# Kernel tuning notes

Measured on AMD Instinct MI355X. Metric: run time of the kernel, lower is better.

## Reference

```python
import jax, jax.numpy as jnp
import numpy as np

B, N, CL = 128, 64, 64


def _lin_params(key, fan_in, fan_out):
    k1, k2 = jax.random.split(key)
    bound = 1.0 / np.sqrt(fan_in)
    w = jax.random.uniform(k1, (fan_in, fan_out), jnp.float32, -bound, bound)
    b = jax.random.uniform(k2, (fan_out,), jnp.float32, -bound, bound)
    return w, b


def setup_inputs() -> dict:
    key = jax.random.key(0)
    ks = jax.random.split(key, 12)
    cl = CL
    se_w1, se_b1 = _lin_params(ks[0], cl, cl)
    se_w2, se_b2 = _lin_params(ks[1], cl, cl)
    sd_w1, sd_b1 = _lin_params(ks[2], cl, 2 * cl)
    sd_w2, sd_b2 = _lin_params(ks[3], 2 * cl, 2 * cl)
    rc_w1, rc_b1 = _lin_params(ks[4], 2 * cl + 1, 2 * cl)
    rc_w2, rc_b2 = _lin_params(ks[5], 2 * cl, 2 * cl)
    rc_w3, rc_b3 = _lin_params(ks[6], 2 * cl, 2 * cl)
    an_w1, an_b1 = _lin_params(ks[7], 2 * cl + 1, cl)
    an_w2, an_b2 = _lin_params(ks[8], cl, 2 * cl)
    s = jax.random.normal(ks[9], (B, N, cl), jnp.float32)
    return dict(s=s,
                se_w1=se_w1, se_b1=se_b1, se_w2=se_w2, se_b2=se_b2,
                sd_w1=sd_w1, sd_b1=sd_b1, sd_w2=sd_w2, sd_b2=sd_b2,
                rc_w1=rc_w1, rc_b1=rc_b1, rc_w2=rc_w2, rc_b2=rc_b2,
                rc_w3=rc_w3, rc_b3=rc_b3,
                an_w1=an_w1, an_b1=an_b1, an_w2=an_w2, an_b2=an_b2)


def reference(s, se_w1, se_b1, se_w2, se_b2,
              sd_w1, sd_b1, sd_w2, sd_b2,
              rc_w1, rc_b1, rc_w2, rc_b2, rc_w3, rc_b3,
              an_w1, an_b1, an_w2, an_b2):
    relu = jax.nn.relu
    # state encoder: [B, N, cl]
    h = relu(relu(s @ se_w1 + se_b1) @ se_w2 + se_b2)
    Bn, Nn, cl = h.shape
    # all-pairs features [B, N, N, cl]
    a1 = jnp.broadcast_to(h[:, :, None, :], (Bn, Nn, Nn, cl))  # object_arg1
    a2 = jnp.broadcast_to(h[:, None, :, :], (Bn, Nn, Nn, cl))  # object_arg2
    dist = (a1[..., 0] - a2[..., 0]) ** 2 + (a1[..., 1] - a2[..., 1]) ** 2
    feat = jnp.concatenate([a1, a2, dist[..., None]], axis=-1)  # [B,N,N,2cl+1]
    rel = relu(relu(relu(feat @ rc_w1 + rc_b1) @ rc_w2 + rc_b2) @ rc_w3 + rc_b3)
    att = jax.nn.sigmoid(relu(feat @ an_w1 + an_b1) @ an_w2 + an_b2)
    rel_dyn = jnp.mean(rel * att, axis=2)  # [B, N, 2cl]
    self_dyn = relu(h @ sd_w1 + sd_b1) @ sd_w2 + sd_b2  # [B, N, 2cl]
    return jnp.mean(self_dyn + rel_dyn, axis=1)  # [B, 2cl]
```

## Files before the change

### kernel.cpp

```cpp
#include <hip/hip_runtime.h>
#include <math.h>

#define TPB 256

typedef unsigned short u16;
typedef __attribute__((ext_vector_type(8))) _Float16 f16x8;
typedef __attribute__((ext_vector_type(4))) float f32x4;

#define BLOB_U16 524288
#define BASE_RC_F32 327680
#define BASE_AN_F32 1376256
#define RC1P_F32 1900544
#define AN1P_F32 2949120
#define WS_NEED_BASES ((size_t)1900544 * 4)
#define WS_NEED_PRE   ((size_t)3473408 * 4)
#define RC1F 0
#define AN1F 16384
#define AN2F 24576
#define RC2F 40960
#define RC3F 73728

#define ENC_NB 512

__device__ __forceinline__ float h2f(u16 b) {
  return (float)__builtin_bit_cast(_Float16, b);
}
__device__ __forceinline__ u16 f2h_rne(float x) {
  return __builtin_bit_cast(u16, (_Float16)x);
}
__device__ __forceinline__ void split_f16(float x, u16& hi, u16& lo) {
  _Float16 h = (_Float16)x;
  hi = __builtin_bit_cast(u16, h);
  lo = __builtin_bit_cast(u16, (_Float16)(x - (float)h));
}
__device__ __forceinline__ unsigned pack_f16(float v0, float v1) {
  auto h = __builtin_amdgcn_cvt_pkrtz(v0, v1);
  return __builtin_bit_cast(unsigned, h);
}

__device__ __forceinline__ void cp_lds(float* dst, const float* src, int nfloats, int tid) {
  const float4* s4 = (const float4*)src;
  float4* d4 = (float4*)dst;
  const int n4 = nfloats >> 2;
  for (int i = tid; i < n4; i += TPB) d4[i] = s4[i];
}
__device__ __forceinline__ void ld4(float r[4], const float* p) {
  float4 v = *(const float4*)p;
  r[0] = v.x; r[1] = v.y; r[2] = v.z; r[3] = v.w;
}
__device__ __forceinline__ void ld2(float r[2], const float* p) {
  float2 v = *(const float2*)p;
  r[0] = v.x; r[1] = v.y;
}

__global__ __launch_bounds__(TPB, 3) void enc_prep_kernel(
    const float* __restrict__ s_in,
    const float* __restrict__ se_w1, const float* __restrict__ se_b1,
    const float* __restrict__ se_w2, const float* __restrict__ se_b2,
    const float* __restrict__ sd_w1, const float* __restrict__ sd_b1,
    const float* __restrict__ sd_w2, const float* __restrict__ sd_b2,
    const float* __restrict__ rc_w1, const float* __restrict__ rc_b1,
    const float* __restrict__ rc_w2, const float* __restrict__ rc_w3,
    const float* __restrict__ an_w1, const float* __restrict__ an_b1,
    const float* __restrict__ an_w2,
    u16* __restrict__ hB, u16* __restrict__ blob,
    float* __restrict__ baseRcG, float* __restrict__ baseAnG,
    float* __restrict__ rc1pG, float* __restrict__ an1pG,
    int do_bases, int do_pre,
    float* __restrict__ out) {
  if (blockIdx.x >= ENC_NB) {
    int idx = (int)(blockIdx.x - ENC_NB) * TPB + threadIdx.x;
    if (idx >= 53248) return;
    int r, base, OK, T; const float* W; int Wld, krow0, twoTerm;
    if (idx < 8192)       { r = idx;         base = RC1F; OK = 8192;  T = 8; W = rc_w1; Wld = 128; krow0 = 64; twoTerm = 1; }
    else if (idx < 12288) { r = idx - 8192;  base = AN1F; OK = 4096;  T = 4; W = an_w1; Wld = 64;  krow0 = 64; twoTerm = 1; }
    else if (idx < 20480) { r = idx - 12288; base = AN2F; OK = 8192;  T = 8; W = an_w2; Wld = 128; krow0 = 0;  twoTerm = 0; }
    else if (idx < 36864) { r = idx - 20480; base = RC2F; OK = 16384; T = 8; W = rc_w2; Wld = 128; krow0 = 0;  twoTerm = 0; }
    else                  { r = idx - 36864; base = RC3F; OK = 16384; T = 8; W = rc_w3; Wld = 128; krow0 = 0;  twoTerm = 0; }
    const int u = r & 7;
    const int lane = (r >> 3) & 63;
    const int ct = r >> 9;
    const int c = (T == 8) ? (ct >> 3) : (ct >> 2);
    const int tg = (T == 8) ? (ct & 7) : (ct & 3);
    const int o = tg * 16 + (lane & 15);
    const int k = c * 32 + (lane >> 4) * 8 + u;
    const float x = W[(krow0 + k) * Wld + o];
    if (twoTerm) {
      u16 hi, lo; split_f16(x, hi, lo);
      blob[base + r] = hi;
      blob[base + OK + r] = lo;
    } else {
      blob[base + r] = f2h_rne(x);
    }
    return;
  }

  __shared__ __align__(16) float sX[1024];
  __shared__ __align__(16) float sH1[1024];
  __shared__ __align__(16) float sT[2048];
  __shared__ __align__(16) float sW[4096];
  __shared__ float sb1[64], sb2[64], sdb1[128], sdb2[128], srb1[128], sab1[64];

  const int tid = threadIdx.x;
  const int lg = tid >> 5;
  const int og = tid & 31;
  const int b = blockIdx.x >> 2;
  const int q = blockIdx.x & 3;
  const int row0 = b * 64 + q * 16;
  const int n0 = lg * 2;

  cp_lds(sX, s_in + row0 * 64, 1024, tid);
  cp_lds(sW, se_w1, 4096, tid);
  if (tid < 64) { sb1[tid] = se_b1[tid]; sb2[tid] = se_b2[tid]; }
  else if (tid < 192) { const int o = tid - 64; sdb1[o] = sd_b1[o]; sdb2[o] = sd_b2[o]; }
  if (tid < 128) srb1[tid] = rc_b1[tid];
  else if (tid < 192) sab1[tid - 128] = an_b1[tid - 128];
  __syncthreads();

  float a2[2][2];
#pragma unroll
  for (int nn = 0; nn < 2; nn++) { a2[nn][0] = 0.f; a2[nn][1] = 0.f; }
  for (int kk = 0; kk < 64; kk += 4) {
    float xr[2][4], wr[4][2];
#pragma unroll
    for (int nn = 0; nn < 2; nn++) ld4(xr[nn], &sX[(n0 + nn) * 64 + kk]);
#pragma unroll
    for (int t = 0; t < 4; t++) ld2(wr[t], &sW[(kk + t) * 64 + og * 2]);
#pragma unroll
    for (int t = 0; t < 4; t++)
#pragma unroll
      for (int nn = 0; nn < 2; nn++) {
        a2[nn][0] = fmaf(xr[nn][t], wr[t][0], a2[nn][0]);
        a2[nn][1] = fmaf(xr[nn][t], wr[t][1], a2[nn][1]);
      }
  }
#pragma unroll
  for (int nn = 0; nn < 2; nn++) {
    float2 v;
    v.x = fmaxf(a2[nn][0] + sb1[og * 2 + 0], 0.f);
    v.y = fmaxf(a2[nn][1] + sb1[og * 2 + 1], 0.f);
    *(float2*)&sH1[(n0 + nn) * 64 + og * 2] = v;
  }
  __syncthreads();
  cp_lds(sW, se_w2, 4096, tid);
  __syncthreads();

#pragma unroll
  for (int nn = 0; nn < 2; nn++) { a2[nn][0] = 0.f; a2[nn][1] = 0.f; }
  for (int kk = 0; kk < 64; kk += 4) {
    float xr[2][4], wr[4][2];
#pragma unroll
    for (int nn = 0; nn < 2; nn++) ld4(xr[nn], &sH1[(n0 + nn) * 64 + kk]);
#pragma unroll
    for (int t = 0; t < 4; t++) ld2(wr[t], &sW[(kk + t) * 64 + og * 2]);
#pragma unroll
    for (int t = 0; t < 4; t++)
#pragma unroll
      for (int nn = 0; nn < 2; nn++) {
        a2[nn][0] = fmaf(xr[nn][t], wr[t][0], a2[nn][0]);
        a2[nn][1] = fmaf(xr[nn][t], wr[t][1], a2[nn][1]);
      }
  }
#pragma unroll
  for (int nn = 0; nn < 2; nn++) {
    float2 v;
    v.x = fmaxf(a2[nn][0] + sb2[og * 2 + 0], 0.f);
    v.y = fmaxf(a2[nn][1] + sb2[og * 2 + 1], 0.f);
    *(float2*)&sX[(n0 + nn) * 64 + og * 2] = v;
    const int off = (row0 + n0 + nn) * 64 + og * 2;
    *(ushort2*)&hB[off] = make_ushort2(f2h_rne(v.x), f2h_rne(v.y));
  }
  __syncthreads();

  float a4[2][4];
#pragma unroll
  for (int nn = 0; nn < 2; nn++)
#pragma unroll
    for (int oo = 0; oo < 4; oo++) a4[nn][oo] = 0.f;
  for (int c = 0; c < 2; c++) {
    cp_lds(sW, sd_w1 + c * 32 * 128, 4096, tid);
    __syncthreads();
    for (int kk = 0; kk < 32; kk += 4) {
      float xr[2][4], wr[4][4];
#pragma unroll
      for (int nn = 0; nn < 2; nn++) ld4(xr[nn], &sX[(n0 + nn) * 64 + c * 32 + kk]);
#pragma unroll
      for (int t = 0; t < 4; t++) ld4(wr[t], &sW[(kk + t) * 128 + og * 4]);
#pragma unroll
      for (int t = 0; t < 4; t++)
#pragma unroll
        for (int nn = 0; nn < 2; nn++)
#pragma unroll
          for (int oo = 0; oo < 4; oo++)
            a4[nn][oo] = fmaf(xr[nn][t], wr[t][oo], a4[nn][oo]);
    }
    __syncthreads();
  }
#pragma unroll
  for (int nn = 0; nn < 2; nn++) {
    float4 v;
    v.x = fmaxf(a4[nn][0] + sdb1[og * 4 + 0], 0.f);
    v.y = fmaxf(a4[nn][1] + sdb1[og * 4 + 1], 0.f);
    v.z = fmaxf(a4[nn][2] + sdb1[og * 4 + 2], 0.f);
    v.w = fmaxf(a4[nn][3] + sdb1[og * 4 + 3], 0.f);
    *(float4*)&sT[(n0 + nn) * 128 + og * 4] = v;
  }
  __syncthreads();

#pragma unroll
  for (int nn = 0; nn < 2; nn++)
#pragma unroll
    for (int oo = 0; oo < 4; oo++) a4[nn][oo] = 0.f;
  for (int c = 0; c < 4; c++) {
    cp_lds(sW, sd_w2 + c * 32 * 128, 4096, tid);
    __syncthreads();
    for (int kk = 0; kk < 32; kk += 4) {
      float xr[2][4], wr[4][4];
#pragma unroll
      for (int nn = 0; nn < 2; nn++) ld4(xr[nn], &sT[(n0 + nn) * 128 + c * 32 + kk]);
#pragma unroll
      for (int t = 0; t < 4; t++) ld4(wr[t], &sW[(kk + t) * 128 + og * 4]);
#pragma unroll
      for (int t = 0; t < 4; t++)
#pragma unroll
        for (int nn = 0; nn < 2; nn++)
#pragma unroll
          for (int oo = 0; oo < 4; oo++)
            a4[nn][oo] = fmaf(xr[nn][t], wr[t][oo], a4[nn][oo]);
    }
    __syncthreads();
  }
  float p[4];
#pragma unroll
  for (int oo = 0; oo < 4; oo++)
    p[oo] = a4[0][oo] + a4[1][oo] + 2.f * sdb2[og * 4 + oo];
  *(float4*)&sH1[lg * 128 + og * 4] = make_float4(p[0], p[1], p[2], p[3]);
  __syncthreads();
  if (tid < 128) {
    float ssum = 0.f;
#pragma unroll
    for (int g = 0; g < 8; g++) ssum += sH1[g * 128 + tid];
    atomicAdd(&out[b * 128 + tid], ssum * (1.0f / 64.0f));
  }

  if (do_bases) {
#pragma unroll
    for (int nn = 0; nn < 2; nn++)
#pragma unroll
      for (int oo = 0; oo < 4; oo++) a4[nn][oo] = 0.f;
    for (int c = 0; c < 2; c++) {
      __syncthreads();
      cp_lds(sW, rc_w1 + c * 32 * 128, 4096, tid);
      __syncthreads();
      for (int kk = 0; kk < 32; kk += 4) {
        float xr[2][4], wr[4][4];
#pragma unroll
        for (int nn = 0; nn < 2; nn++) ld4(xr[nn], &sX[(n0 + nn) * 64 + c * 32 + kk]);
#pragma unroll
        for (int t = 0; t < 4; t++) ld4(wr[t], &sW[(kk + t) * 128 + og * 4]);
#pragma unroll
        for (int t = 0; t < 4; t++)
#pragma unroll
          for (int nn = 0; nn < 2; nn++)
#pragma unroll
            for (int oo = 0; oo < 4; oo++)
              a4[nn][oo] = fmaf(xr[nn][t], wr[t][oo], a4[nn][oo]);
      }
    }
#pragma unroll
    for (int nn = 0; nn < 2; nn++) {
      float4 v;
      v.x = a4[nn][0] + srb1[og * 4 + 0];
      v.y = a4[nn][1] + srb1[og * 4 + 1];
      v.z = a4[nn][2] + srb1[og * 4 + 2];
      v.w = a4[nn][3] + srb1[og * 4 + 3];
      *(float4*)&baseRcG[(size_t)(row0 + n0 + nn) * 128 + og * 4] = v;
    }
    __syncthreads();
    cp_lds(sW, an_w1, 4096, tid);
    __syncthreads();
#pragma unroll
    for (int nn = 0; nn < 2; nn++) { a2[nn][0] = 0.f; a2[nn][1] = 0.f; }
    for (int kk = 0; kk < 64; kk += 4) {
      float xr[2][4], wr[4][2];
#pragma unroll
      for (int nn = 0; nn < 2; nn++) ld4(xr[nn], &sX[(n0 + nn) * 64 + kk]);
#pragma unroll
      for (int t = 0; t < 4; t++) ld2(wr[t], &sW[(kk + t) * 64 + og * 2]);
#pragma unroll
      for (int t = 0; t < 4; t++)
#pragma unroll
        for (int nn = 0; nn < 2; nn++) {
          a2[nn][0] = fmaf(xr[nn][t], wr[t][0], a2[nn][0]);
          a2[nn][1] = fmaf(xr[nn][t], wr[t][1], a2[nn][1]);
        }
    }
#pragma unroll
    for (int nn = 0; nn < 2; nn++) {
      float2 v;
      v.x = a2[nn][0] + sab1[og * 2 + 0];
      v.y = a2[nn][1] + sab1[og * 2 + 1];
      *(float2*)&baseAnG[(size_t)(row0 + n0 + nn) * 64 + og * 2] = v;
    }
  }

  if (do_pre) {
#pragma unroll
    for (int nn = 0; nn < 2; nn++)
#pragma unroll
      for (int oo = 0; oo < 4; oo++) a4[nn][oo] = 0.f;
    for (int c = 0; c < 2; c++) {
      __syncthreads();
      cp_lds(sW, rc_w1 + (64 + c * 32) * 128, 4096, tid);
      __syncthreads();
      for (int kk = 0; kk < 32; kk += 4) {
        float xr[2][4], wr[4][4];
#pragma unroll
        for (int nn = 0; nn < 2; nn++) ld4(xr[nn], &sX[(n0 + nn) * 64 + c * 32 + kk]);
#pragma unroll
        for (int t = 0; t < 4; t++) ld4(wr[t], &sW[(kk + t) * 128 + og * 4]);
#pragma unroll
        for (int t = 0; t < 4; t++)
#pragma unroll
          for (int nn = 0; nn < 2; nn++)
#pragma unroll
            for (int oo = 0; oo < 4; oo++)
              a4[nn][oo] = fmaf(xr[nn][t], wr[t][oo], a4[nn][oo]);
      }
    }
#pragma unroll
    for (int nn = 0; nn < 2; nn++) {
      const int jl = q * 16 + n0 + nn;
      const int addr = ((b * 8 + (og >> 2)) * 4 + (jl >> 4)) * 256 +
                       ((og & 3) * 16 + (jl & 15)) * 4;
      *(float4*)&rc1pG[addr] = make_float4(a4[nn][0], a4[nn][1], a4[nn][2], a4[nn][3]);
    }
    __syncthreads();
    cp_lds(sW, an_w1 + 64 * 64, 4096, tid);
    __syncthreads();
#pragma unroll
    for (int nn = 0; nn < 2; nn++) { a2[nn][0] = 0.f; a2[nn][1] = 0.f; }
    for (int kk = 0; kk < 64; kk += 4) {
      float xr[2][4], wr[4][2];
#pragma unroll
      for (int nn = 0; nn < 2; nn++) ld4(xr[nn], &sX[(n0 + nn) * 64 + kk]);
#pragma unroll
      for (int t = 0; t < 4; t++) ld2(wr[t], &sW[(kk + t) * 64 + og * 2]);
#pragma unroll
      for (int t = 0; t < 4; t++)
#pragma unroll
        for (int nn = 0; nn < 2; nn++) {
          a2[nn][0] = fmaf(xr[nn][t], wr[t][0], a2[nn][0]);
          a2[nn][1] = fmaf(xr[nn][t], wr[t][1], a2[nn][1]);
        }
    }
#pragma unroll
    for (int nn = 0; nn < 2; nn++) {
      const int jl = q * 16 + n0 + nn;
      const int addr = ((b * 4 + (og >> 3)) * 4 + (jl >> 4)) * 256 +
                       (((og >> 1) & 3) * 16 + (jl & 15)) * 4 + (og & 1) * 2;
      *(float2*)&an1pG[addr] = make_float2(a2[nn][0], a2[nn][1]);
    }
  }
}

template<int MT, int NCHUNK, int RSG, int TILES>
__device__ __forceinline__ void run_layer1(f32x4 (&acc)[MT][4],
    const u16* __restrict__ blobL,
    const u16* __restrict__ sB, int tg0, int quad, int l15) {
  const int lane = quad * 16 + l15;
#pragma unroll
  for (int c = 0; c < NCHUNK; ++c) {
    f16x8 Ah[MT];
#pragma unroll
    for (int t = 0; t < MT; ++t)
      Ah[t] = *(const f16x8*)(blobL + ((c * TILES + tg0 + t) * 64 + lane) * 8);
    const int slot = (4 * c + quad) ^ (l15 & 7);
    f16x8 Bh[4];
#pragma unroll
    for (int s = 0; s < 4; ++s)
      Bh[s] = *(const f16x8*)&sB[(16 * s + l15) * (RSG * 8) + slot * 8];
#pragma unroll
    for (int t = 0; t < MT; ++t)
#pragma unroll
      for (int s = 0; s < 4; ++s)
        acc[t][s] = __builtin_amdgcn_mfma_f32_16x16x32_f16(Ah[t], Bh[s], acc[t][s], 0, 0, 0);
  }
}

template<int MT, int RSG>
__device__ __forceinline__ void store_acts_pk(const f32x4 (&acc)[MT][4],
                                              u16* dst, int o0, int quad, int l15) {
#pragma unroll
  for (int t = 0; t < MT; ++t) {
    const int ob = o0 + 16 * t + quad * 4;
    const int slot = (ob >> 3) ^ (l15 & 7);
    const int e = ob & 7;
#pragma unroll
    for (int s = 0; s < 4; ++s) {
      const int j = 16 * s + l15;
      uint2 pk;
      pk.x = pack_f16(fmaxf(acc[t][s][0], 0.f), fmaxf(acc[t][s][1], 0.f));
      pk.y = pack_f16(fmaxf(acc[t][s][2], 0.f), fmaxf(acc[t][s][3], 0.f));
      *(uint2*)&dst[j * (RSG * 8) + slot * 8 + e] = pk;
    }
  }
}

__global__ __launch_bounds__(TPB, 4) void pair_mfma_kernel(
    const u16* __restrict__ hB, const u16* __restrict__ blob,
    const float* __restrict__ baseRcG, const float* __restrict__ baseAnG,
    const float* __restrict__ rc1pG, const float* __restrict__ an1pG,
    int has_bases, int has_pre,
    const float* __restrict__ rc_w1, const float* __restrict__ rc_b1,
    const float* __restrict__ rc_b2, const float* __restrict__ rc_b3,
    const float* __restrict__ an_w1, const float* __restrict__ an_b1,
    const float* __restrict__ an_b2,
    float* __restrict__ out) {
  __shared__ __align__(16) u16 sAct[64 * 128];
  __shared__ __align__(16) u16 sAn[64 * 64];
  __shared__ float sHi[64], sDist[64];
  __shared__ float sBaseRc[128], sBaseAn[64], sW1d[128], sAnd[64];
  __shared__ float sB2[128], sB3[128], sAb2[128], sRed[128];

  const int tid = threadIdx.x;
  const int w = tid >> 6, lane = tid & 63;
  const int quad = lane >> 4, l15 = lane & 15;
  const int b = blockIdx.x >> 6, i = blockIdx.x & 63;
  const int o0 = w * 32;
  const int o0a = w * 16;

  f32x4 accR[2][4];
  f32x4 accN[1][4];

  if (has_pre) {
    if (tid < 128) {
      sW1d[tid] = rc_w1[128 * 128 + tid];
      sB2[tid] = rc_b2[tid]; sB3[tid] = rc_b3[tid]; sAb2[tid] = an_b2[tid];
    } else if (tid < 192) {
      sAnd[tid - 128] = an_w1[128 * 64 + (tid - 128)];
    } else {
      const int j = tid - 192;
      const float hi0 = h2f(hB[(b * 64 + i) * 64 + 0]);
      const float hi1 = h2f(hB[(b * 64 + i) * 64 + 1]);
      const ushort2 hj = *(const ushort2*)&hB[(b * 64 + j) * 64];
      const float d0 = hi0 - h2f(hj.x), d1 = hi1 - h2f(hj.y);
      sDist[j] = d0 * d0 + d1 * d1;
    }
    if (tid < 32)
      ((float4*)sBaseRc)[tid] = ((const float4*)(baseRcG + (size_t)(b * 64 + i) * 128))[tid];
    else if (tid < 48)
      ((float4*)sBaseAn)[tid - 32] = ((const float4*)(baseAnG + (size_t)(b * 64 + i) * 64))[tid - 32];
    __syncthreads();

    float bbR[2][4], wwR[2][4], bbN[4], wwN[4];
#pragma unroll
    for (int t = 0; t < 2; ++t) {
      ld4(bbR[t], &sBaseRc[o0 + 16 * t + quad * 4]);
      ld4(wwR[t], &sW1d[o0 + 16 * t + quad * 4]);
    }
    ld4(bbN, &sBaseAn[o0a + quad * 4]);
    ld4(wwN, &sAnd[o0a + quad * 4]);
    const float* pR = rc1pG + (size_t)(b * 8 + 2 * w) * 1024 + lane * 4;
    const float* pA = an1pG + (size_t)(b * 4 + w) * 1024 + lane * 4;
#pragma unroll
    for (int s = 0; s < 4; ++s) {
      const float dj = sDist[16 * s + l15];
#pragma unroll
      for (int t = 0; t < 2; ++t) {
        const float4 pre = *(const float4*)(pR + t * 1024 + s * 256);
        f32x4 a;
        a[0] = pre.x + fmaf(dj, wwR[t][0], bbR[t][0]);
        a[1] = pre.y + fmaf(dj, wwR[t][1], bbR[t][1]);
        a[2] = pre.z + fmaf(dj, wwR[t][2], bbR[t][2]);
        a[3] = pre.w + fmaf(dj, wwR[t][3], bbR[t][3]);
        accR[t][s] = a;
      }
      const float4 pre = *(const float4*)(pA + s * 256);
      f32x4 a;
      a[0] = pre.x + fmaf(dj, wwN[0], bbN[0]);
      a[1] = pre.y + fmaf(dj, wwN[1], bbN[1]);
      a[2] = pre.z + fmaf(dj, wwN[2], bbN[2]);
      a[3] = pre.w + fmaf(dj, wwN[3], bbN[3]);
      accN[0][s] = a;
    }
    store_acts_pk<1, 8>(accN, sAn, o0a, quad, l15);
    store_acts_pk<2, 16>(accR, sAct, o0, quad, l15);
    __syncthreads();
  } else {
    {
      const float4* srcJ = (const float4*)(hB + b * 4096);
      for (int idx = tid; idx < 512; idx += TPB) {
        const int row = idx >> 3, g = idx & 7;
        *(float4*)&sAct[row * 128 + ((g ^ (row & 7)) * 8)] = srcJ[idx];
      }
    }
    if (has_bases) {
      const float4* bR = (const float4*)(baseRcG + (size_t)(b * 64 + i) * 128);
      const float4* bA = (const float4*)(baseAnG + (size_t)(b * 64 + i) * 64);
      if (tid < 32) ((float4*)sBaseRc)[tid] = bR[tid];
      else if (tid < 48) ((float4*)sBaseAn)[tid - 32] = bA[tid - 32];
    }
    if (tid < 64) sHi[tid] = h2f(hB[(b * 64 + i) * 64 + tid]);
    if (tid < 128) {
      sW1d[tid] = rc_w1[128 * 128 + tid];
      sB2[tid] = rc_b2[tid]; sB3[tid] = rc_b3[tid]; sAb2[tid] = an_b2[tid];
    } else if (tid < 192) {
      sAnd[tid - 128] = an_w1[128 * 64 + (tid - 128)];
    }
    __syncthreads();
    if (!has_bases) {
      if (tid < 128) {
        float acc = rc_b1[tid];
        for (int k = 0; k < 64; ++k) acc = fmaf(sHi[k], rc_w1[k * 128 + tid], acc);
        sBaseRc[tid] = acc;
      } else if (tid < 192) {
        const int o = tid - 128;
        float acc = an_b1[o];
        for (int k = 0; k < 64; ++k) acc = fmaf(sHi[k], an_w1[k * 64 + o], acc);
        sBaseAn[o] = acc;
      }
    }
    if (tid >= 192) {
      const int j = tid - 192;
      const int base = j * 128 + ((0 ^ (j & 7)) * 8);
      const float d0 = sHi[0] - h2f(sAct[base + 0]);
      const float d1 = sHi[1] - h2f(sAct[base + 1]);
      sDist[j] = d0 * d0 + d1 * d1;
    }
    __syncthreads();

    {
      float bbR[2][4], wwR[2][4], bbN[4], wwN[4];
#pragma unroll
      for (int t = 0; t < 2; ++t) {
        ld4(bbR[t], &sBaseRc[o0 + 16 * t + quad * 4]);
        ld4(wwR[t], &sW1d[o0 + 16 * t + quad * 4]);
      }
      ld4(bbN, &sBaseAn[o0a + quad * 4]);
      ld4(wwN, &sAnd[o0a + quad * 4]);
#pragma unroll
      for (int s = 0; s < 4; ++s) {
        const float dj = sDist[16 * s + l15];
#pragma unroll
        for (int t = 0; t < 2; ++t) {
          f32x4 a;
#pragma unroll
          for (int r = 0; r < 4; ++r) a[r] = fmaf(dj, wwR[t][r], bbR[t][r]);
          accR[t][s] = a;
        }
        f32x4 a;
#pragma unroll
        for (int r = 0; r < 4; ++r) a[r] = fmaf(dj, wwN[r], bbN[r]);
        accN[0][s] = a;
      }
    }
    {
      const int lane64 = quad * 16 + l15;
#pragma unroll
      for (int c = 0; c < 2; ++c) {
        f16x8 Ah[2], Al[2], AhN, AlN;
#pragma unroll
        for (int t = 0; t < 2; ++t) {
          const u16* p = blob + RC1F + ((c * 8 + 2 * w + t) * 64 + lane64) * 8;
          Ah[t] = *(const f16x8*)p;
          Al[t] = *(const f16x8*)(p + 8192);
        }
        {
          const u16* p = blob + AN1F + ((c * 4 + w) * 64 + lane64) * 8;
          AhN = *(const f16x8*)p;
          AlN = *(const f16x8*)(p + 4096);
        }
        const int slot = (4 * c + quad) ^ (l15 & 7);
        f16x8 Bh[4];
#pragma unroll
        for (int s = 0; s < 4; ++s)
          Bh[s] = *(const f16x8*)&sAct[(16 * s + l15) * 128 + slot * 8];
#pragma unroll
        for (int s = 0; s < 4; ++s) {
#pragma unroll
          for (int t = 0; t < 2; ++t) {
            f32x4 a = accR[t][s];
            a = __builtin_amdgcn_mfma_f32_16x16x32_f16(Ah[t], Bh[s], a, 0, 0, 0);
            a = __builtin_amdgcn_mfma_f32_16x16x32_f16(Al[t], Bh[s], a, 0, 0, 0);
            accR[t][s] = a;
          }
          f32x4 a = accN[0][s];
          a = __builtin_amdgcn_mfma_f32_16x16x32_f16(AhN, Bh[s], a, 0, 0, 0);
          a = __builtin_amdgcn_mfma_f32_16x16x32_f16(AlN, Bh[s], a, 0, 0, 0);
          accN[0][s] = a;
        }
      }
    }
    store_acts_pk<1, 8>(accN, sAn, o0a, quad, l15);
    __syncthreads();
    store_acts_pk<2, 16>(accR, sAct, o0, quad, l15);
    __syncthreads();
  }

  {
    float bb[2][4];
#pragma unroll
    for (int t = 0; t < 2; ++t) ld4(bb[t], &sB2[o0 + 16 * t + quad * 4]);
#pragma unroll
    for (int t = 0; t < 2; ++t)
#pragma unroll
      for (int s = 0; s < 4; ++s) {
        f32x4 a;
#pragma unroll
        for (int r = 0; r < 4; ++r) a[r] = bb[t][r];
        accR[t][s] = a;
      }
  }
  run_layer1<2, 4, 16, 8>(accR, blob + RC2F, sAct, 2 * w, quad, l15);
  __syncthreads();
  store_acts_pk<2, 16>(accR, sAct, o0, quad, l15);
  __syncthreads();

  f32x4 accT[2][4];
  {
    float bb[2][4];
#pragma unroll
    for (int t = 0; t < 2; ++t) ld4(bb[t], &sAb2[o0 + 16 * t + quad * 4]);
#pragma unroll
    for (int t = 0; t < 2; ++t)
#pragma unroll
      for (int s = 0; s < 4; ++s) {
        f32x4 a;
#pragma unroll
        for (int r = 0; r < 4; ++r) a[r] = bb[t][r];
        accT[t][s] = a;
      }
  }
  run_layer1<2, 2, 8, 8>(accT, blob + AN2F, sAn, 2 * w, quad, l15);
  float att[2][4][4];
#pragma unroll
  for (int t = 0; t < 2; ++t)
#pragma unroll
    for (int s = 0; s < 4; ++s)
#pragma unroll
      for (int r = 0; r < 4; ++r)
        att[t][s][r] = __builtin_amdgcn_rcpf(1.0f + __expf(-accT[t][s][r]));

  {
    float bb[2][4];
#pragma unroll
    for (int t = 0; t < 2; ++t) ld4(bb[t], &sB3[o0 + 16 * t + quad * 4]);
#pragma unroll
    for (int t = 0; t < 2; ++t)
#pragma unroll
      for (int s = 0; s < 4; ++s) {
        f32x4 a;
#pragma unroll
        for (int r = 0; r < 4; ++r) a[r] = bb[t][r];
        accR[t][s] = a;
      }
  }
  run_layer1<2, 4, 16, 8>(accR, blob + RC3F, sAct, 2 * w, quad, l15);
  float ps[2][4] = {{0.f, 0.f, 0.f, 0.f}, {0.f, 0.f, 0.f, 0.f}};
#pragma unroll
  for (int t = 0; t < 2; ++t)
#pragma unroll
    for (int s = 0; s < 4; ++s)
#pragma unroll
      for (int r = 0; r < 4; ++r) {
        const float rel = fmaxf(accR[t][s][r], 0.f);
        ps[t][r] = fmaf(rel, att[t][s][r], ps[t][r]);
      }
#pragma unroll
  for (int t = 0; t < 2; ++t)
#pragma unroll
    for (int r = 0; r < 4; ++r) {
      float v = ps[t][r];
      v += __shfl_xor(v, 1, 64);
      v += __shfl_xor(v, 2, 64);
      v += __shfl_xor(v, 4, 64);
      v += __shfl_xor(v, 8, 64);
      ps[t][r] = v;
    }
  if (l15 == 0) {
#pragma unroll
    for (int t = 0; t < 2; ++t)
#pragma unroll
      for (int r = 0; r < 4; ++r)
        sRed[o0 + 16 * t + quad * 4 + r] = ps[t][r];
  }
  __syncthreads();
  if (tid < 128)
    atomicAdd(&out[b * 128 + tid], sRed[tid] * (1.0f / 4096.0f));
}

extern "C" void kernel_launch(void* const* d_in, const int* in_sizes, int n_in,
                              void* d_out, int out_size, void* d_ws, size_t ws_size,
                              hipStream_t stream) {
  const float* s     = (const float*)d_in[0];
  const float* se_w1 = (const float*)d_in[1];
  const float* se_b1 = (const float*)d_in[2];
  const float* se_w2 = (const float*)d_in[3];
  const float* se_b2 = (const float*)d_in[4];
  const float* sd_w1 = (const float*)d_in[5];
  const float* sd_b1 = (const float*)d_in[6];
  const float* sd_w2 = (const float*)d_in[7];
  const float* sd_b2 = (const float*)d_in[8];
  const float* rc_w1 = (const float*)d_in[9];
  const float* rc_b1 = (const float*)d_in[10];
  const float* rc_w2 = (const float*)d_in[11];
  const float* rc_b2 = (const float*)d_in[12];
  const float* rc_w3 = (const float*)d_in[13];
  const float* rc_b3 = (const float*)d_in[14];
  const float* an_w1 = (const float*)d_in[15];
  const float* an_b1 = (const float*)d_in[16];
  const float* an_w2 = (const float*)d_in[17];
  const float* an_b2 = (const float*)d_in[18];
  float* out = (float*)d_out;
  u16* hB   = (u16*)d_ws;
  u16* blob = hB + BLOB_U16;
  float* baseRcG = (float*)d_ws + BASE_RC_F32;
  float* baseAnG = (float*)d_ws + BASE_AN_F32;
  float* rc1pG   = (float*)d_ws + RC1P_F32;
  float* an1pG   = (float*)d_ws + AN1P_F32;
  const int has_pre   = (ws_size >= WS_NEED_PRE) ? 1 : 0;
  const int has_bases = (ws_size >= WS_NEED_BASES) ? 1 : 0;
  (void)n_in; (void)in_sizes;

  hipMemsetAsync(d_out, 0, (size_t)out_size * sizeof(float), stream);
  enc_prep_kernel<<<ENC_NB + 208, TPB, 0, stream>>>(s, se_w1, se_b1, se_w2, se_b2,
                                           sd_w1, sd_b1, sd_w2, sd_b2,
                                           rc_w1, rc_b1, rc_w2, rc_w3,
                                           an_w1, an_b1, an_w2,
                                           hB, blob, baseRcG, baseAnG, rc1pG, an1pG,
                                           has_bases, has_pre, out);
  pair_mfma_kernel<<<8192, TPB, 0, stream>>>(hB, blob, baseRcG, baseAnG, rc1pG, an1pG,
                                             has_bases, has_pre,
                                             rc_w1, rc_b1, rc_b2, rc_b3,
                                             an_w1, an_b1, an_b2, out);
}
```

Baseline: 191.5 us.

## Rewrite encoder prep kernel with split-f16 MFMA, one block per batch

The encoder/precompute kernel previously ran scalar fp32 FMAs over 512 blocks of 16 rows each. It now uses one block per batch (128 blocks) and runs every small matmul on f16 MFMA with a hi/lo split (three MFMAs per tile) to keep near-fp32 accuracy. Weights are converted into swizzled hi/lo f16 layouts in LDS inside each block, and the self-dynamics reduction moves to wave shuffles. This trades scalar ALU work for matrix-core work, but with only 128 blocks per-block weight conversion is repeated and parallelism is lower, which may limit the gain on a kernel that is small next to the pair kernel.

```diff
diff --git a/kernel.cpp b/kernel.cpp
--- a/kernel.cpp
+++ b/kernel.cpp
@@ -4,6 +4,7 @@
 #define TPB 256
 
 typedef unsigned short u16;
+typedef unsigned int u32;
 typedef __attribute__((ext_vector_type(8))) _Float16 f16x8;
 typedef __attribute__((ext_vector_type(4))) float f32x4;
 
@@ -20,7 +21,7 @@
 #define RC2F 40960
 #define RC3F 73728
 
-#define ENC_NB 512
+#define ENC_BLOCKS 128
 
 __device__ __forceinline__ float h2f(u16 b) {
   return (float)__builtin_bit_cast(_Float16, b);
@@ -37,23 +38,132 @@
   auto h = __builtin_amdgcn_cvt_pkrtz(v0, v1);
   return __builtin_bit_cast(unsigned, h);
 }
-
-__device__ __forceinline__ void cp_lds(float* dst, const float* src, int nfloats, int tid) {
-  const float4* s4 = (const float4*)src;
-  float4* d4 = (float4*)dst;
-  const int n4 = nfloats >> 2;
-  for (int i = tid; i < n4; i += TPB) d4[i] = s4[i];
+__device__ __forceinline__ void split4(const float4 v, uint2& H, uint2& L) {
+  _Float16 h0 = (_Float16)v.x, h1 = (_Float16)v.y;
+  _Float16 h2 = (_Float16)v.z, h3 = (_Float16)v.w;
+  _Float16 l0 = (_Float16)(v.x - (float)h0), l1 = (_Float16)(v.y - (float)h1);
+  _Float16 l2 = (_Float16)(v.z - (float)h2), l3 = (_Float16)(v.w - (float)h3);
+  H.x = (u32)__builtin_bit_cast(u16, h0) | ((u32)__builtin_bit_cast(u16, h1) << 16);
+  H.y = (u32)__builtin_bit_cast(u16, h2) | ((u32)__builtin_bit_cast(u16, h3) << 16);
+  L.x = (u32)__builtin_bit_cast(u16, l0) | ((u32)__builtin_bit_cast(u16, l1) << 16);
+  L.y = (u32)__builtin_bit_cast(u16, l2) | ((u32)__builtin_bit_cast(u16, l3) << 16);
 }
 __device__ __forceinline__ void ld4(float r[4], const float* p) {
   float4 v = *(const float4*)p;
   r[0] = v.x; r[1] = v.y; r[2] = v.z; r[3] = v.w;
 }
-__device__ __forceinline__ void ld2(float r[2], const float* p) {
-  float2 v = *(const float2*)p;
-  r[0] = v.x; r[1] = v.y;
-}
-
-__global__ __launch_bounds__(TPB, 3) void enc_prep_kernel(
+
+template<int KDIM, int ODIM>
+__device__ __forceinline__ void prep_w(u16* __restrict__ hi, u16* __restrict__ lo,
+                                       const float* __restrict__ W, int tid) {
+  constexpr int N = KDIM * ODIM / TPB;
+  constexpr int OSH = (ODIM == 128) ? 7 : 6;
+#pragma unroll
+  for (int base = 0; base < N; base += 16) {
+    float v[16];
+#pragma unroll
+    for (int i = 0; i < 16; ++i) v[i] = W[(base + i) * TPB + tid];
+#pragma unroll
+    for (int i = 0; i < 16; ++i) {
+      const int e = (base + i) * TPB + tid;
+      const int k = e >> OSH, o = e & (ODIM - 1);
+      const int idx = ((k >> 5) * (ODIM >> 4) + (o >> 4)) * 512 +
+                      ((k >> 3) & 3) * 128 + (o & 15) * 8 + (k & 7);
+      const float x = v[i];
+      const _Float16 h = (_Float16)x;
+      hi[idx] = __builtin_bit_cast(u16, h);
+      lo[idx] = __builtin_bit_cast(u16, (_Float16)(x - (float)h));
+    }
+  }
+}
+
+template<int MT, int NCHUNK, int RSG, int TILES>
+__device__ __forceinline__ void run3(f32x4 (&acc)[MT][4],
+    const u16* __restrict__ wHi, const u16* __restrict__ wLo,
+    const u16* __restrict__ bHi, const u16* __restrict__ bLo,
+    int tg0, int quad, int l15) {
+  const int lane = quad * 16 + l15;
+#pragma unroll
+  for (int c = 0; c < NCHUNK; ++c) {
+    f16x8 Ah[MT], Al[MT];
+#pragma unroll
+    for (int t = 0; t < MT; ++t) {
+      const int off = ((c * TILES + tg0 + t) * 64 + lane) * 8;
+      Ah[t] = *(const f16x8*)(wHi + off);
+      Al[t] = *(const f16x8*)(wLo + off);
+    }
+    const int slot = (4 * c + quad) ^ (l15 & 7);
+    f16x8 Bh[4], Bl[4];
+#pragma unroll
+    for (int s = 0; s < 4; ++s) {
+      const int off = (16 * s + l15) * (RSG * 8) + slot * 8;
+      Bh[s] = *(const f16x8*)(bHi + off);
+      Bl[s] = *(const f16x8*)(bLo + off);
+    }
+#pragma unroll
+    for (int t = 0; t < MT; ++t)
+#pragma unroll
+      for (int s = 0; s < 4; ++s) {
+        f32x4 a = acc[t][s];
+        a = __builtin_amdgcn_mfma_f32_16x16x32_f16(Ah[t], Bh[s], a, 0, 0, 0);
+        a = __builtin_amdgcn_mfma_f32_16x16x32_f16(Al[t], Bh[s], a, 0, 0, 0);
+        a = __builtin_amdgcn_mfma_f32_16x16x32_f16(Ah[t], Bl[s], a, 0, 0, 0);
+        acc[t][s] = a;
+      }
+  }
+}
+
+template<int MT, int RSG>
+__device__ __forceinline__ void store_hl(const f32x4 (&acc)[MT][4],
+    u16* __restrict__ dH, u16* __restrict__ dL, int o0, int quad, int l15) {
+#pragma unroll
+  for (int t = 0; t < MT; ++t) {
+    const int ob = o0 + 16 * t + quad * 4;
+    const int slot = (ob >> 3) ^ (l15 & 7);
+    const int e = ob & 7;
+#pragma unroll
+    for (int s = 0; s < 4; ++s) {
+      const int j = 16 * s + l15;
+      float4 v = make_float4(fmaxf(acc[t][s][0], 0.f), fmaxf(acc[t][s][1], 0.f),
+                             fmaxf(acc[t][s][2], 0.f), fmaxf(acc[t][s][3], 0.f));
+      uint2 H, L;
+      split4(v, H, L);
+      *(uint2*)&dH[j * (RSG * 8) + slot * 8 + e] = H;
+      *(uint2*)&dL[j * (RSG * 8) + slot * 8 + e] = L;
+    }
+  }
+}
+
+template<int MT>
+__device__ __forceinline__ void initb(f32x4 (&acc)[MT][4], const float* bias,
+                                      int o0, int quad) {
+#pragma unroll
+  for (int t = 0; t < MT; ++t) {
+    float bb[4];
+    ld4(bb, &bias[o0 + 16 * t + quad * 4]);
+#pragma unroll
+    for (int s = 0; s < 4; ++s) {
+      f32x4 a;
+#pragma unroll
+      for (int r = 0; r < 4; ++r) a[r] = bb[r];
+      acc[t][s] = a;
+    }
+  }
+}
+template<int MT>
+__device__ __forceinline__ void zeroa(f32x4 (&acc)[MT][4]) {
+#pragma unroll
+  for (int t = 0; t < MT; ++t)
+#pragma unroll
+    for (int s = 0; s < 4; ++s) {
+      f32x4 a;
+#pragma unroll
+      for (int r = 0; r < 4; ++r) a[r] = 0.f;
+      acc[t][s] = a;
+    }
+}
+
+__global__ __launch_bounds__(TPB, 1) void enc_prep_kernel(
     const float* __restrict__ s_in,
     const float* __restrict__ se_w1, const float* __restrict__ se_b1,
     const float* __restrict__ se_w2, const float* __restrict__ se_b2,
@@ -68,8 +178,8 @@
     float* __restrict__ rc1pG, float* __restrict__ an1pG,
     int do_bases, int do_pre,
     float* __restrict__ out) {
-  if (blockIdx.x >= ENC_NB) {
-    int idx = (int)(blockIdx.x - ENC_NB) * TPB + threadIdx.x;
+  if (blockIdx.x >= ENC_BLOCKS) {
+    int idx = (int)(blockIdx.x - ENC_BLOCKS) * TPB + threadIdx.x;
     if (idx >= 53248) return;
     int r, base, OK, T; const float* W; int Wld, krow0, twoTerm;
     if (idx < 8192)       { r = idx;         base = RC1F; OK = 8192;  T = 8; W = rc_w1; Wld = 128; krow0 = 64; twoTerm = 1; }
@@ -95,271 +205,153 @@
     return;
   }
 
-  __shared__ __align__(16) float sX[1024];
-  __shared__ __align__(16) float sH1[1024];
-  __shared__ __align__(16) float sT[2048];
-  __shared__ __align__(16) float sW[4096];
-  __shared__ float sb1[64], sb2[64], sdb1[128], sdb2[128], srb1[128], sab1[64];
+  __shared__ __align__(16) u16 sW[32768];
+  __shared__ __align__(16) u16 sB0h[4096], sB0l[4096];
+  __shared__ __align__(16) u16 sB1h[4096], sB1l[4096];
+  __shared__ __align__(16) u16 sB2h[8192], sB2l[8192];
+  __shared__ float sb[576];
+  __shared__ float sRed[128];
 
   const int tid = threadIdx.x;
-  const int lg = tid >> 5;
-  const int og = tid & 31;
-  const int b = blockIdx.x >> 2;
-  const int q = blockIdx.x & 3;
-  const int row0 = b * 64 + q * 16;
-  const int n0 = lg * 2;
-
-  cp_lds(sX, s_in + row0 * 64, 1024, tid);
-  cp_lds(sW, se_w1, 4096, tid);
-  if (tid < 64) { sb1[tid] = se_b1[tid]; sb2[tid] = se_b2[tid]; }
-  else if (tid < 192) { const int o = tid - 64; sdb1[o] = sd_b1[o]; sdb2[o] = sd_b2[o]; }
-  if (tid < 128) srb1[tid] = rc_b1[tid];
-  else if (tid < 192) sab1[tid - 128] = an_b1[tid - 128];
-  __syncthreads();
-
-  float a2[2][2];
-#pragma unroll
-  for (int nn = 0; nn < 2; nn++) { a2[nn][0] = 0.f; a2[nn][1] = 0.f; }
-  for (int kk = 0; kk < 64; kk += 4) {
-    float xr[2][4], wr[4][2];
-#pragma unroll
-    for (int nn = 0; nn < 2; nn++) ld4(xr[nn], &sX[(n0 + nn) * 64 + kk]);
-#pragma unroll
-    for (int t = 0; t < 4; t++) ld2(wr[t], &sW[(kk + t) * 64 + og * 2]);
-#pragma unroll
-    for (int t = 0; t < 4; t++)
-#pragma unroll
-      for (int nn = 0; nn < 2; nn++) {
-        a2[nn][0] = fmaf(xr[nn][t], wr[t][0], a2[nn][0]);
-        a2[nn][1] = fmaf(xr[nn][t], wr[t][1], a2[nn][1]);
-      }
-  }
-#pragma unroll
-  for (int nn = 0; nn < 2; nn++) {
-    float2 v;
-    v.x = fmaxf(a2[nn][0] + sb1[og * 2 + 0], 0.f);
-    v.y = fmaxf(a2[nn][1] + sb1[og * 2 + 1], 0.f);
-    *(float2*)&sH1[(n0 + nn) * 64 + og * 2] = v;
-  }
-  __syncthreads();
-  cp_lds(sW, se_w2, 4096, tid);
-  __syncthreads();
-
-#pragma unroll
-  for (int nn = 0; nn < 2; nn++) { a2[nn][0] = 0.f; a2[nn][1] = 0.f; }
-  for (int kk = 0; kk < 64; kk += 4) {
-    float xr[2][4], wr[4][2];
-#pragma unroll
-    for (int nn = 0; nn < 2; nn++) ld4(xr[nn], &sH1[(n0 + nn) * 64 + kk]);
-#pragma unroll
-    for (int t = 0; t < 4; t++) ld2(wr[t], &sW[(kk + t) * 64 + og * 2]);
-#pragma unroll
-    for (int t = 0; t < 4; t++)
-#pragma unroll
-      for (int nn = 0; nn < 2; nn++) {
-        a2[nn][0] = fmaf(xr[nn][t], wr[t][0], a2[nn][0]);
-        a2[nn][1] = fmaf(xr[nn][t], wr[t][1], a2[nn][1]);
-      }
-  }
-#pragma unroll
-  for (int nn = 0; nn < 2; nn++) {
-    float2 v;
-    v.x = fmaxf(a2[nn][0] + sb2[og * 2 + 0], 0.f);
-    v.y = fmaxf(a2[nn][1] + sb2[og * 2 + 1], 0.f);
-    *(float2*)&sX[(n0 + nn) * 64 + og * 2] = v;
-    const int off = (row0 + n0 + nn) * 64 + og * 2;
-    *(ushort2*)&hB[off] = make_ushort2(f2h_rne(v.x), f2h_rne(v.y));
-  }
-  __syncthreads();
-
-  float a4[2][4];
-#pragma unroll
-  for (int nn = 0; nn < 2; nn++)
-#pragma unroll
-    for (int oo = 0; oo < 4; oo++) a4[nn][oo] = 0.f;
-  for (int c = 0; c < 2; c++) {
-    cp_lds(sW, sd_w1 + c * 32 * 128, 4096, tid);
-    __syncthreads();
-    for (int kk = 0; kk < 32; kk += 4) {
-      float xr[2][4], wr[4][4];
-#pragma unroll
-      for (int nn = 0; nn < 2; nn++) ld4(xr[nn], &sX[(n0 + nn) * 64 + c * 32 + kk]);
-#pragma unroll
-      for (int t = 0; t < 4; t++) ld4(wr[t], &sW[(kk + t) * 128 + og * 4]);
-#pragma unroll
-      for (int t = 0; t < 4; t++)
-#pragma unroll
-        for (int nn = 0; nn < 2; nn++)
-#pragma unroll
-          for (int oo = 0; oo < 4; oo++)
-            a4[nn][oo] = fmaf(xr[nn][t], wr[t][oo], a4[nn][oo]);
-    }
-    __syncthreads();
-  }
-#pragma unroll
-  for (int nn = 0; nn < 2; nn++) {
-    float4 v;
-    v.x = fmaxf(a4[nn][0] + sdb1[og * 4 + 0], 0.f);
-    v.y = fmaxf(a4[nn][1] + sdb1[og * 4 + 1], 0.f);
-    v.z = fmaxf(a4[nn][2] + sdb1[og * 4 + 2], 0.f);
-    v.w = fmaxf(a4[nn][3] + sdb1[og * 4 + 3], 0.f);
-    *(float4*)&sT[(n0 + nn) * 128 + og * 4] = v;
-  }
-  __syncthreads();
-
-#pragma unroll
-  for (int nn = 0; nn < 2; nn++)
-#pragma unroll
-    for (int oo = 0; oo < 4; oo++) a4[nn][oo] = 0.f;
-  for (int c = 0; c < 4; c++) {
-    cp_lds(sW, sd_w2 + c * 32 * 128, 4096, tid);
-    __syncthreads();
-    for (int kk = 0; kk < 32; kk += 4) {
-      float xr[2][4], wr[4][4];
-#pragma unroll
-      for (int nn = 0; nn < 2; nn++) ld4(xr[nn], &sT[(n0 + nn) * 128 + c * 32 + kk]);
-#pragma unroll
-      for (int t = 0; t < 4; t++) ld4(wr[t], &sW[(kk + t) * 128 + og * 4]);
-#pragma unroll
-      for (int t = 0; t < 4; t++)
-#pragma unroll
-        for (int nn = 0; nn < 2; nn++)
-#pragma unroll
-          for (int oo = 0; oo < 4; oo++)
-            a4[nn][oo] = fmaf(xr[nn][t], wr[t][oo], a4[nn][oo]);
-    }
-    __syncthreads();
-  }
-  float p[4];
-#pragma unroll
-  for (int oo = 0; oo < 4; oo++)
-    p[oo] = a4[0][oo] + a4[1][oo] + 2.f * sdb2[og * 4 + oo];
-  *(float4*)&sH1[lg * 128 + og * 4] = make_float4(p[0], p[1], p[2], p[3]);
-  __syncthreads();
-  if (tid < 128) {
-    float ssum = 0.f;
-#pragma unroll
-    for (int g = 0; g < 8; g++) ssum += sH1[g * 128 + tid];
-    atomicAdd(&out[b * 128 + tid], ssum * (1.0f / 64.0f));
-  }
+  const int w = tid >> 6, lane = tid & 63;
+  const int quad = lane >> 4, l15 = lane & 15;
+  const int b = blockIdx.x;
+  const int o0 = w * 32;
+  const int o0a = w * 16;
+
+  if (tid < 64) {
+    sb[tid] = se_b1[tid]; sb[64 + tid] = se_b2[tid]; sb[512 + tid] = an_b1[tid];
+  } else if (tid < 192) {
+    const int o = tid - 64;
+    sb[128 + o] = sd_b1[o]; sb[256 + o] = sd_b2[o]; sb[384 + o] = rc_b1[o];
+  }
+
+  {
+    const float* sp = s_in + (size_t)b * 4096;
+#pragma unroll
+    for (int i = 0; i < 2; ++i) {
+      const int idx = tid + i * 256;
+      const int j = idx >> 3, g = idx & 7;
+      const float4 p0 = *(const float4*)(sp + j * 64 + g * 8);
+      const float4 p1 = *(const float4*)(sp + j * 64 + g * 8 + 4);
+      uint2 H0, L0, H1, L1;
+      split4(p0, H0, L0);
+      split4(p1, H1, L1);
+      const int d = j * 64 + ((g ^ (j & 7)) * 8);
+      *(uint4*)&sB0h[d] = make_uint4(H0.x, H0.y, H1.x, H1.y);
+      *(uint4*)&sB0l[d] = make_uint4(L0.x, L0.y, L1.x, L1.y);
+    }
+  }
+
+  prep_w<64, 64>(sW + 0, sW + 4096, se_w1, tid);
+  prep_w<64, 64>(sW + 8192, sW + 12288, se_w2, tid);
+  prep_w<64, 128>(sW + 16384, sW + 24576, sd_w1, tid);
+  __syncthreads();
+
+  f32x4 a64[1][4];
+  f32x4 a128[2][4];
+
+  initb<1>(a64, sb + 0, o0a, quad);
+  run3<1, 2, 8, 4>(a64, sW + 0, sW + 4096, sB0h, sB0l, w, quad, l15);
+  store_hl<1, 8>(a64, sB1h, sB1l, o0a, quad, l15);
+  __syncthreads();
+
+  initb<1>(a64, sb + 64, o0a, quad);
+  run3<1, 2, 8, 4>(a64, sW + 8192, sW + 12288, sB1h, sB1l, w, quad, l15);
+  store_hl<1, 8>(a64, sB0h, sB0l, o0a, quad, l15);
+  __syncthreads();
+
+#pragma unroll
+  for (int i = 0; i < 2; ++i) {
+    const int idx = tid + i * 256;
+    const int j = idx >> 3, g = idx & 7;
+    const uint4 v = *(const uint4*)&sB0h[j * 64 + ((g ^ (j & 7)) * 8)];
+    *(uint4*)&hB[(size_t)(b * 64 + j) * 64 + g * 8] = v;
+  }
+
+  initb<2>(a128, sb + 128, o0, quad);
+  run3<2, 2, 8, 8>(a128, sW + 16384, sW + 24576, sB0h, sB0l, 2 * w, quad, l15);
+  store_hl<2, 16>(a128, sB2h, sB2l, o0, quad, l15);
+  __syncthreads();
+
+  prep_w<128, 128>(sW + 0, sW + 16384, sd_w2, tid);
+  __syncthreads();
+
+  zeroa<2>(a128);
+  run3<2, 4, 16, 8>(a128, sW + 0, sW + 16384, sB2h, sB2l, 2 * w, quad, l15);
+  {
+    float ps[2][4];
+#pragma unroll
+    for (int t = 0; t < 2; ++t)
+#pragma unroll
+      for (int r = 0; r < 4; ++r) {
+        float v = a128[t][0][r] + a128[t][1][r] + a128[t][2][r] + a128[t][3][r];
+        v += __shfl_xor(v, 1, 64);
+        v += __shfl_xor(v, 2, 64);
+        v += __shfl_xor(v, 4, 64);
+        v += __shfl_xor(v, 8, 64);
+        ps[t][r] = v;
+      }
+    if (l15 == 0) {
+#pragma unroll
+      for (int t = 0; t < 2; ++t)
+#pragma unroll
+        for (int r = 0; r < 4; ++r)
+          sRed[o0 + 16 * t + quad * 4 + r] = ps[t][r];
+    }
+  }
+  __syncthreads();
+  if (tid < 128)
+    atomicAdd(&out[b * 128 + tid], sRed[tid] * (1.0f / 64.0f) + sb[256 + tid]);
+
+  if (do_bases) prep_w<64, 128>(sW + 0, sW + 8192, rc_w1, tid);
+  if (do_pre)   prep_w<64, 128>(sW + 16384, sW + 24576, rc_w1 + 64 * 128, tid);
+  __syncthreads();
 
   if (do_bases) {
-#pragma unroll
-    for (int nn = 0; nn < 2; nn++)
-#pragma unroll
-      for (int oo = 0; oo < 4; oo++) a4[nn][oo] = 0.f;
-    for (int c = 0; c < 2; c++) {
-      __syncthreads();
-      cp_lds(sW, rc_w1 + c * 32 * 128, 4096, tid);
-      __syncthreads();
-      for (int kk = 0; kk < 32; kk += 4) {
-        float xr[2][4], wr[4][4];
-#pragma unroll
-        for (int nn = 0; nn < 2; nn++) ld4(xr[nn], &sX[(n0 + nn) * 64 + c * 32 + kk]);
-#pragma unroll
-        for (int t = 0; t < 4; t++) ld4(wr[t], &sW[(kk + t) * 128 + og * 4]);
-#pragma unroll
-        for (int t = 0; t < 4; t++)
-#pragma unroll
-          for (int nn = 0; nn < 2; nn++)
-#pragma unroll
-            for (int oo = 0; oo < 4; oo++)
-              a4[nn][oo] = fmaf(xr[nn][t], wr[t][oo], a4[nn][oo]);
-      }
-    }
-#pragma unroll
-    for (int nn = 0; nn < 2; nn++) {
-      float4 v;
-      v.x = a4[nn][0] + srb1[og * 4 + 0];
-      v.y = a4[nn][1] + srb1[og * 4 + 1];
-      v.z = a4[nn][2] + srb1[og * 4 + 2];
-      v.w = a4[nn][3] + srb1[og * 4 + 3];
-      *(float4*)&baseRcG[(size_t)(row0 + n0 + nn) * 128 + og * 4] = v;
-    }
-    __syncthreads();
-    cp_lds(sW, an_w1, 4096, tid);
-    __syncthreads();
-#pragma unroll
-    for (int nn = 0; nn < 2; nn++) { a2[nn][0] = 0.f; a2[nn][1] = 0.f; }
-    for (int kk = 0; kk < 64; kk += 4) {
-      float xr[2][4], wr[4][2];
-#pragma unroll
-      for (int nn = 0; nn < 2; nn++) ld4(xr[nn], &sX[(n0 + nn) * 64 + kk]);
-#pragma unroll
-      for (int t = 0; t < 4; t++) ld2(wr[t], &sW[(kk + t) * 64 + og * 2]);
-#pragma unroll
-      for (int t = 0; t < 4; t++)
-#pragma unroll
-        for (int nn = 0; nn < 2; nn++) {
-          a2[nn][0] = fmaf(xr[nn][t], wr[t][0], a2[nn][0]);
-          a2[nn][1] = fmaf(xr[nn][t], wr[t][1], a2[nn][1]);
-        }
-    }
-#pragma unroll
-    for (int nn = 0; nn < 2; nn++) {
-      float2 v;
-      v.x = a2[nn][0] + sab1[og * 2 + 0];
-      v.y = a2[nn][1] + sab1[og * 2 + 1];
-      *(float2*)&baseAnG[(size_t)(row0 + n0 + nn) * 64 + og * 2] = v;
-    }
-  }
-
+    initb<2>(a128, sb + 384, o0, quad);
+    run3<2, 2, 8, 8>(a128, sW + 0, sW + 8192, sB0h, sB0l, 2 * w, quad, l15);
+#pragma unroll
+    for (int t = 0; t < 2; ++t)
+#pragma unroll
+      for (int s = 0; s < 4; ++s) {
+        float4 v = make_float4(a128[t][s][0], a128[t][s][1], a128[t][s][2], a128[t][s][3]);
+        *(float4*)&baseRcG[(size_t)(b * 64 + 16 * s + l15) * 128 + o0 + 16 * t + quad * 4] = v;
+      }
+  }
   if (do_pre) {
-#pragma unroll
-    for (int nn = 0; nn < 2; nn++)
-#pragma unroll
-      for (int oo = 0; oo < 4; oo++) a4[nn][oo] = 0.f;
-    for (int c = 0; c < 2; c++) {
-      __syncthreads();
-      cp_lds(sW, rc_w1 + (64 + c * 32) * 128, 4096, tid);
-      __syncthreads();
-      for (int kk = 0; kk < 32; kk += 4) {
-        float xr[2][4], wr[4][4];
-#pragma unroll
-        for (int nn = 0; nn < 2; nn++) ld4(xr[nn], &sX[(n0 + nn) * 64 + c * 32 + kk]);
-#pragma unroll
-        for (int t = 0; t < 4; t++) ld4(wr[t], &sW[(kk + t) * 128 + og * 4]);
-#pragma unroll
-        for (int t = 0; t < 4; t++)
-#pragma unroll
-          for (int nn = 0; nn < 2; nn++)
-#pragma unroll
-            for (int oo = 0; oo < 4; oo++)
-              a4[nn][oo] = fmaf(xr[nn][t], wr[t][oo], a4[nn][oo]);
-      }
-    }
-#pragma unroll
-    for (int nn = 0; nn < 2; nn++) {
-      const int jl = q * 16 + n0 + nn;
-      const int addr = ((b * 8 + (og >> 2)) * 4 + (jl >> 4)) * 256 +
-                       ((og & 3) * 16 + (jl & 15)) * 4;
-      *(float4*)&rc1pG[addr] = make_float4(a4[nn][0], a4[nn][1], a4[nn][2], a4[nn][3]);
-    }
-    __syncthreads();
-    cp_lds(sW, an_w1 + 64 * 64, 4096, tid);
-    __syncthreads();
-#pragma unroll
-    for (int nn = 0; nn < 2; nn++) { a2[nn][0] = 0.f; a2[nn][1] = 0.f; }
-    for (int kk = 0; kk < 64; kk += 4) {
-      float xr[2][4], wr[4][2];
-#pragma unroll
-      for (int nn = 0; nn < 2; nn++) ld4(xr[nn], &sX[(n0 + nn) * 64 + kk]);
-#pragma unroll
-      for (int t = 0; t < 4; t++) ld2(wr[t], &sW[(kk + t) * 64 + og * 2]);
-#pragma unroll
-      for (int t = 0; t < 4; t++)
-#pragma unroll
-        for (int nn = 0; nn < 2; nn++) {
-          a2[nn][0] = fmaf(xr[nn][t], wr[t][0], a2[nn][0]);
-          a2[nn][1] = fmaf(xr[nn][t], wr[t][1], a2[nn][1]);
-        }
-    }
-#pragma unroll
-    for (int nn = 0; nn < 2; nn++) {
-      const int jl = q * 16 + n0 + nn;
-      const int addr = ((b * 4 + (og >> 3)) * 4 + (jl >> 4)) * 256 +
-                       (((og >> 1) & 3) * 16 + (jl & 15)) * 4 + (og & 1) * 2;
-      *(float2*)&an1pG[addr] = make_float2(a2[nn][0], a2[nn][1]);
+    zeroa<2>(a128);
+    run3<2, 2, 8, 8>(a128, sW + 16384, sW + 24576, sB0h, sB0l, 2 * w, quad, l15);
+#pragma unroll
+    for (int t = 0; t < 2; ++t)
+#pragma unroll
+      for (int s = 0; s < 4; ++s) {
+        float4 v = make_float4(a128[t][s][0], a128[t][s][1], a128[t][s][2], a128[t][s][3]);
+        *(float4*)&rc1pG[(size_t)((b * 8 + 2 * w + t) * 4 + s) * 256 + lane * 4] = v;
+      }
+  }
+  __syncthreads();
+
+  if (do_bases) prep_w<64, 64>(sW + 0, sW + 4096, an_w1, tid);
+  if (do_pre)   prep_w<64, 64>(sW + 8192, sW + 12288, an_w1 + 64 * 64, tid);
+  __syncthreads();
+
+  if (do_bases) {
+    initb<1>(a64, sb + 512, o0a, quad);
+    run3<1, 2, 8, 4>(a64, sW + 0, sW + 4096, sB0h, sB0l, w, quad, l15);
+#pragma unroll
+    for (int s = 0; s < 4; ++s) {
+      float4 v = make_float4(a64[0][s][0], a64[0][s][1], a64[0][s][2], a64[0][s][3]);
+      *(float4*)&baseAnG[(size_t)(b * 64 + 16 * s + l15) * 64 + o0a + quad * 4] = v;
+    }
+  }
+  if (do_pre) {
+    zeroa<1>(a64);
+    run3<1, 2, 8, 4>(a64, sW + 8192, sW + 12288, sB0h, sB0l, w, quad, l15);
+#pragma unroll
+    for (int s = 0; s < 4; ++s) {
+      float4 v = make_float4(a64[0][s][0], a64[0][s][1], a64[0][s][2], a64[0][s][3]);
+      *(float4*)&an1pG[(size_t)((b * 4 + w) * 4 + s) * 256 + lane * 4] = v;
     }
   }
 }
@@ -724,7 +716,7 @@
   (void)n_in; (void)in_sizes;
 
   hipMemsetAsync(d_out, 0, (size_t)out_size * sizeof(float), stream);
-  enc_prep_kernel<<<ENC_NB + 208, TPB, 0, stream>>>(s, se_w1, se_b1, se_w2, se_b2,
+  enc_prep_kernel<<<ENC_BLOCKS + 208, TPB, 0, stream>>>(s, se_w1, se_b1, se_w2, se_b2,
                                            sd_w1, sd_b1, sd_w2, sd_b2,
                                            rc_w1, rc_b1, rc_w2, rc_w3,
                                            an_w1, an_b1, an_w2,
```

Measured after the change: 180.3 us. 5.8% less time.
